# Kernel optimization log

Measured on AMD Instinct MI355X. Metric: run time of the kernel, lower is better.

Reference implementation:

```python
import jax, jax.numpy as jnp
import numpy as np
from jax.scipy.linalg import solve_triangular


def setup_inputs() -> dict:
    key = jax.random.key(0)
    k1, k2 = jax.random.split(key)
    # [K classes, N per class, D features] training embeddings
    src_seq = jax.random.normal(k1, (256, 64, 128), dtype=jnp.float32)
    # [M, D] vectors to project and pairwise-score (clustering inner loop)
    test = jax.random.normal(k2, (8192, 128), dtype=jnp.float32)
    return {"src_seq": src_seq, "test": test}


def _fit_model(src_seq):
    # Faithful port of compute_scatter_matrices + fit_model.
    # S_w, S_b are symmetric PSD, so solve(S_w,S_b) eig is replaced by the
    # equivalent (and differentiable) generalized symmetric eig via Cholesky
    # whitening; A_inverse and psi are invariant to eigvec scaling/order.
    K, N, D = src_seq.shape
    count = K * N
    mean_per_class = src_seq.mean(axis=1)            # [K, D]
    mean = src_seq.mean(axis=(0, 1))                 # [D]
    diff_w = src_seq - mean_per_class[:, None, :]    # [K, N, D]
    diff_b = mean_per_class - mean                   # [K, D]
    S_w = jnp.einsum('knd,kne->de', diff_w, diff_w) / count   # [D, D]
    S_b = (N * jnp.einsum('kd,ke->de', diff_b, diff_b)) / count

    L = jnp.linalg.cholesky(S_w)                     # S_w = L L^T
    # Msym = L^{-1} S_b L^{-T}
    tmp = solve_triangular(L, S_b, lower=True)
    Msym = solve_triangular(L, tmp.T, lower=True).T
    Msym = 0.5 * (Msym + Msym.T)
    evals, U = jnp.linalg.eigh(Msym)
    W = solve_triangular(L, U, lower=True, trans=1)  # W = L^{-T} U, eigvecs of S_w^{-1} S_b

    lambda_b = jnp.sum(W * (S_b @ W), axis=0)        # diag(W^T S_b W)
    lambda_w = jnp.sum(W * (S_w @ W), axis=0)        # diag(W^T S_w W)
    n = float(N)
    # A = W^{-T} diag(sqrt(n/(n-1) * lambda_w))  =>  A^{-1} = diag(1/sqrt(.)) W^T
    A_inverse = (1.0 / jnp.sqrt(n / (n - 1.0) * lambda_w))[:, None] * W.T
    psi = jnp.clip((n - 1.0) / n * (lambda_b / lambda_w) - 1.0 / n, 0.0)
    return A_inverse, mean, psi


def reference(src_seq, test):
    A_inverse, mean, psi = _fit_model(src_seq)
    # latent = A_inverse @ (x - mean), batched over rows
    latent = (test - mean) @ A_inverse.T             # [M, D]
    # Pairwise single-vector probability (calculate_probability_single),
    # vectorized over all (i, j) pairs, in log space:
    # log p(i,j) = -(v_i - v_j)^T diag(psi) (v_i - v_j)
    #             - 0.5 * (D*log(2*pi) + log(||psi||_F))
    D = latent.shape[1]
    q = jnp.sum(psi * latent * latent, axis=1)       # [M]
    G = (latent * psi) @ latent.T                    # [M, M]
    maha = q[:, None] + q[None, :] - 2.0 * G         # [M, M]
    log_div = 0.5 * (D * jnp.log(2.0 * jnp.pi) + jnp.log(jnp.linalg.norm(psi)))
    return -maha - log_div                           # [M, M] pairwise log-prob
```

## Files before the change

### kernel.cpp

```cpp
#include <hip/hip_runtime.h>
#include <math.h>


#define D 128
#define NCLS 256
#define NPC 64
#define MTEST 8192
#define COUNT (NCLS*NPC)

#define fMC    0
#define fMEAN  16384
#define fSCAL  16640
#define fMAT   32768
#define fSWRAW 442368
#define fPART  458752
#define fU     458752
#define fV     983040
#define fQ     1507328
#define fBBF   1515520

#define sP   0
#define sSB  1
#define sP2  2
#define sP3  3
#define sP4  4
#define sZ   5
#define sM1  6
#define sMm  7
#define sC2  8
#define sC4  9
#define sXH  10
#define sT2  11
#define sT3  12
#define sT4  13
#define sT5  14
#define sT10 15
#define sT15 16
#define sT20 17
#define sG0  18
#define sF   23
#define sA1  24

using short8 = __attribute__((ext_vector_type(8))) short;
using f32x4  = __attribute__((ext_vector_type(4))) float;

__device__ inline unsigned short f2bf(float f) {
  unsigned u = __float_as_uint(f);
  unsigned r = u + 0x7FFFu + ((u >> 16) & 1u);
  return (unsigned short)(r >> 16);
}
__device__ inline float bf2f(unsigned short h) {
  return __uint_as_float(((unsigned)h) << 16);
}
__device__ inline float valU(const unsigned short* m, int idx) {
  return bf2f(m[idx]) + bf2f(m[idx + 16384]);
}
__device__ inline void storeDual(unsigned short* m, int idx, float g) {
  unsigned short hb = f2bf(g);
  m[idx] = hb;
  m[16384 + idx] = f2bf(g - bf2f(hb));
}
__device__ inline unsigned short* MS(float* ws, int m) {
  return (unsigned short*)(ws + fMAT) + (size_t)m * 32768;
}
__device__ inline const unsigned short* MSc(const float* ws, int m) {
  return (const unsigned short*)(ws + fMAT) + (size_t)m * 32768;
}

__global__ __launch_bounds__(256) void k_gt_partial(const float* __restrict__ X, float* __restrict__ ws) {
  __shared__ unsigned short xt[128 * 256];
  int b = blockIdx.x, tid = threadIdx.x;
  const float* Xc = X + b * 256 * D;
  for (int idx = tid; idx < 256 * D; idx += 256) {
    int s = idx >> 7, d = idx & 127;
    unsigned byte = ((unsigned)(d * 512 + s * 2)) ^ (((unsigned)(d & 7)) << 4);
    *(unsigned short*)((char*)xt + byte) = f2bf(Xc[idx]);
  }
  {
    int d = tid & 127;
    for (int cc = (tid >> 7); cc < 4; cc += 2) {
      const float* p = Xc + cc * 64 * D + d;
// ... 28 lines not shown
  }
  float* outp = ws + fPART + b * 16384;
  #pragma unroll
  for (int mt = 0; mt < 4; mt++)
    #pragma unroll
    for (int nt = 0; nt < 4; nt++)
      #pragma unroll
      for (int r = 0; r < 4; r++) {
        int row = wr + mt * 16 + (lane >> 4) * 4 + r;
        int col = wc + nt * 16 + (lane & 15);
        outp[row * 128 + col] = acc[mt][nt][r];
      }
}

__global__ void k_reduce(float* __restrict__ ws) {
  int tid = threadIdx.x;
  int idx = blockIdx.x * 256 + tid;
  const float* part = ws + fPART;
  float s = 0.f;
  #pragma unroll 8
  for (int p = 0; p < 64; p++) s += part[p * 16384 + idx];
  ws[fSWRAW + idx] = s;
  if (blockIdx.x == 0 && tid < 128) {
    const unsigned short* McT = (const unsigned short*)ws;
    float m = 0.f;
    for (int k = 0; k < 256; k++) m += bf2f(McT[tid * 256 + k]);
    ws[fMEAN + tid] = m * (1.0f / 256.0f);
  }
}

__global__ __launch_bounds__(256) void k_sb(float* __restrict__ ws) {
  __shared__ float red[4];
  const unsigned short* Mc = (const unsigned short*)ws;
  const float* mv = ws + fMEAN;
  const float* swraw = ws + fSWRAW;
  unsigned short* SB = MS(ws, sSB);
  float* scal = ws + fSCAL;
  int tid = threadIdx.x, b = blockIdx.x;
  int w = tid >> 6, lane = tid & 63;
  int brow = b * 32, wcol = w * 32;
  f32x4 acc[2][2] = {};
  for (int ks = 0; ks < 8; ks++) {
    int kb = ks * 32 + (lane >> 4) * 8;
    short8 af[2], bfv[2];
    #pragma unroll
    for (int mt = 0; mt < 2; mt++) {
      int r = brow + mt * 16 + (lane & 15);
      af[mt] = *(const short8*)(Mc + r * 256 + kb);
    }
    #pragma unroll
    for (int nt = 0; nt < 2; nt++) {
      int c = wcol + nt * 16 + (lane & 15);
      bfv[nt] = *(const short8*)(Mc + c * 256 + kb);
    }
    #pragma unroll
    for (int mt = 0; mt < 2; mt++)
      #pragma unroll
      for (int nt = 0; nt < 2; nt++)
        acc[mt][nt] = __builtin_amdgcn_mfma_f32_16x16x32_bf16(af[mt], bfv[nt], acc[mt][nt], 0, 0, 0);
  }
  float tsum = 0.f;
  #pragma unroll
  for (int mt = 0; mt < 2; mt++)
    #pragma unroll
    for (int nt = 0; nt < 2; nt++)
      #pragma unroll
      for (int r = 0; r < 4; r++) {
        int row = brow + mt * 16 + (lane >> 4) * 4 + r;
        int col = wcol + nt * 16 + (lane & 15);
        int idx = row * 128 + col;
        float g = acc[mt][nt][r] * (1.0f / 256.0f) - mv[row] * mv[col];
        storeDual(SB, idx, g);
        if (row == col)
          tsum += swraw[row * 129] * (1.0f / COUNT) - g - mv[row] * mv[row];
      }
  #pragma unroll
  for (int off = 32; off > 0; off >>= 1) tsum += __shfl_down(tsum, off);
  if (lane == 0) red[w] = tsum;
  __syncthreads();
  if (tid == 0) scal[64 + b] = red[0] + red[1] + red[2] + red[3];
}

__global__ __launch_bounds__(256) void k_swfin(float* __restrict__ ws) {
  float* scal = ws + fSCAL;
  float inv_s = 128.0f / (scal[64] + scal[65] + scal[66] + scal[67]);
  const float* mv = ws + fMEAN;
  const float* swraw = ws + fSWRAW;
  const unsigned short* SB = MS(ws, sSB);
  unsigned short* P = MS(ws, sP);
  int gid = blockIdx.x * 256 + threadIdx.x;
  #pragma unroll
  for (int t = 0; t < 4; t++) {
    int idx = gid * 4 + t;
    int row = idx >> 7, col = idx & 127;
    float sb = valU(SB, idx);
    float s = (swraw[idx] * (1.0f / COUNT) - sb - mv[row] * mv[col]) * inv_s;
    storeDual(P, idx, s - ((row == col) ? 1.0f : 0.0f));
  }
  if (blockIdx.x == 0 && threadIdx.x == 0) {
    scal[1] = inv_s;
    scal[7] = 0.984375f * inv_s;
  }
}

__device__ __forceinline__ void mm_body(
    const unsigned short* __restrict__ A, const unsigned short* __restrict__ B,
    unsigned short* __restrict__ C, const unsigned short* __restrict__ E1,
    float alpha, const float* alpha_ptr, float beta, float delta,
    float* scal, int trace_slot, unsigned short* outBf, int b, float* red) {
  int tid = threadIdx.x;
  int w = tid >> 6, lane = tid & 63;
  int brow = b * 32, wcol = w * 32;
  f32x4 acc[2][2] = {};
  #pragma unroll
  for (int ks = 0; ks < 4; ks++) {
    int kb = ks * 32 + (lane >> 4) * 8;
    short8 ah[2], al[2], bh[2], bl[2];
    #pragma unroll
    for (int mt = 0; mt < 2; mt++) {
      int r = brow + mt * 16 + (lane & 15);
      ah[mt] = *(const short8*)(A + r * 128 + kb);
      al[mt] = *(const short8*)(A + 16384 + r * 128 + kb);
    }
    #pragma unroll
    for (int nt = 0; nt < 2; nt++) {
      int c = wcol + nt * 16 + (lane & 15);
      bh[nt] = *(const short8*)(B + c * 128 + kb);
      bl[nt] = *(const short8*)(B + 16384 + c * 128 + kb);
    }
    #pragma unroll
    for (int mt = 0; mt < 2; mt++)
      #pragma unroll
      for (int nt = 0; nt < 2; nt++) {
        f32x4 a0 = acc[mt][nt];
        a0 = __builtin_amdgcn_mfma_f32_16x16x32_bf16(ah[mt], bh[nt], a0, 0, 0, 0);
        a0 = __builtin_amdgcn_mfma_f32_16x16x32_bf16(al[mt], bh[nt], a0, 0, 0, 0);
        a0 = __builtin_amdgcn_mfma_f32_16x16x32_bf16(ah[mt], bl[nt], a0, 0, 0, 0);
        acc[mt][nt] = a0;
      }
  }
  float aeff = alpha * (alpha_ptr ? alpha_ptr[0] : 1.0f);
  float tsum = 0.0f;
  #pragma unroll
  for (int mt = 0; mt < 2; mt++)
    #pragma unroll
    for (int nt = 0; nt < 2; nt++)
      #pragma unroll
      for (int r = 0; r < 4; r++) {
        int row = brow + mt * 16 + (lane >> 4) * 4 + r;
        int col = wcol + nt * 16 + (lane & 15);
        int idx = row * 128 + col;
        float g = acc[mt][nt][r] * aeff;
        if (E1) g += beta * (bf2f(E1[idx]) + bf2f(E1[16384 + idx]));
        if (row == col) g += delta;
        if (outBf) outBf[idx] = f2bf(g);
        else storeDual(C, idx, g);
        tsum += g * g;
      }
  if (trace_slot >= 0) {
    #pragma unroll
    for (int off = 32; off > 0; off >>= 1) tsum += __shfl_down(tsum, off);
    if (lane == 0) red[w] = tsum;
    __syncthreads();
    if (tid == 0) scal[trace_slot + b] = red[0] + red[1] + red[2] + red[3];
  }
}

__global__ __launch_bounds__(256) void k_mm(
    const unsigned short* A, const unsigned short* B, unsigned short* C,
    const unsigned short* E1, float alpha, const float* alpha_ptr,
    float beta, float delta, float* scal, int trace_slot, unsigned short* outBf) {
  __shared__ float red[4];
  mm_body(A, B, C, E1, alpha, alpha_ptr, beta, delta, scal, trace_slot, outBf, blockIdx.x, red);
}

__global__ __launch_bounds__(256) void k_mm2(
    const unsigned short* A0, const unsigned short* B0, unsigned short* C0,
    const unsigned short* E0, float al0, float be0, float de0,
    const unsigned short* A1, const unsigned short* B1, unsigned short* C1,
    const unsigned short* E1, float al1, float be1, float de1,
    float* scal, int tslot1) {
  __shared__ float red[4];
  int b = blockIdx.x & 3;
  if (blockIdx.x < 4)
    mm_body(A0, B0, C0, E0, al0, nullptr, be0, de0, scal, -1, nullptr, b, red);
  else
    mm_body(A1, B1, C1, E1, al1, nullptr, be1, de1, scal, tslot1, nullptr, b, red);
}

__global__ __launch_bounds__(256) void k_p56z(float* __restrict__ ws) {
  __shared__ float cj[7];
  __shared__ float bt[7];
  float* scal = ws + fSCAL;
  const unsigned short *P = MSc(ws, sP), *P2 = MSc(ws, sP2),
    *P3 = MSc(ws, sP3), *P4 = MSc(ws, sP4);
  unsigned short* Z = MS(ws, sZ);
  int tid = threadIdx.x, b = blockIdx.x;
  float trP8 = scal[60] + scal[61] + scal[62] + scal[63];
  float a = 1.05f * sqrtf(sqrtf(sqrtf(fmaxf(trP8, 1e-30f))));
  a = fminf(a, 0.95f);
  if (tid < 7) {
    const float PI = 3.14159265358979f;
    float s = 0.f;
    for (int i = 0; i < 64; i++) {
      float th = (i + 0.5f) * (PI / 64.0f);
      float x = cosf(th);
      s += (1.0f / sqrtf(1.0f + a * x)) * cosf((float)tid * th);
    }
    cj[tid] = s * (2.0f / 64.0f);
  }
  __syncthreads();
  if (tid == 0) {
    float c0h = 0.5f * cj[0];
    float m0 = c0h - cj[2] + cj[4] - cj[6];
    float m1 = cj[1] - 3.0f * cj[3] + 5.0f * cj[5];
    float m2 = 2.0f * cj[2] - 8.0f * cj[4] + 18.0f * cj[6];
    float m3 = 4.0f * cj[3] - 20.0f * cj[5];
    float m4 = 8.0f * cj[4] - 48.0f * cj[6];
    float m5 = 16.0f * cj[5];
    float m6 = 32.0f * cj[6];
    float ia = 1.0f / a;
    float p = 1.f;
    bt[0] = m0;
    p *= ia; bt[1] = m1 * p;
    p *= ia; bt[2] = m2 * p;
    p *= ia; bt[3] = m3 * p;
    p *= ia; bt[4] = m4 * p;
    p *= ia; bt[5] = m5 * p;
    p *= ia; bt[6] = m6 * p;
  }
  __syncthreads();
  int w = tid >> 6, lane = tid & 63;
  int brow = b * 32, wcol = w * 32;
  f32x4 a5[2][2] = {}, a6[2][2] = {};
  #pragma unroll
  for (int ks = 0; ks < 4; ks++) {
    int kb = ks * 32 + (lane >> 4) * 8;
// ... 33 lines not shown
    #pragma unroll
    for (int nt = 0; nt < 2; nt++)
      #pragma unroll
      for (int r = 0; r < 4; r++) {
        int row = brow + mt * 16 + (lane >> 4) * 4 + r;
        int col = wcol + nt * 16 + (lane & 15);
        int idx = row * 128 + col;
        float dg = (row == col) ? 1.0f : 0.0f;
        float z = bt[0] * dg + bt[1] * valU(P, idx) + bt[2] * valU(P2, idx) +
                  bt[3] * valU(P3, idx) + bt[4] * valU(P4, idx) +
                  bt[5] * a5[mt][nt][r] + bt[6] * a6[mt][nt][r];
        storeDual(Z, idx, z);
      }
}

__device__ inline void interval_cs(const float* scal, float* c0o, float* iho) {
  float trM8 = scal[68] + scal[69] + scal[70] + scal[71];
  float Lam = 1.03f * sqrtf(sqrtf(sqrtf(fmaxf(trM8, 1e-37f))));
  float lo = -0.02f * Lam, hi = Lam;
  *c0o = 0.5f * (hi + lo);
  *iho = 1.0f / (0.5f * (hi - lo));
}

__global__ __launch_bounds__(256) void k_xh_t2(float* __restrict__ ws) {
  __shared__ float cs[2];
  float* scal = ws + fSCAL;
  if (threadIdx.x == 0) {
    float c0, ih;
    interval_cs(scal, &c0, &ih);
    cs[0] = c0; cs[1] = ih;
  }
  __syncthreads();
  float c0 = cs[0], ih = cs[1];
  float a2 = 2.0f * ih * ih, b2 = -4.0f * c0 * ih * ih, g2 = 2.0f * c0 * c0 * ih * ih - 1.0f;
  const unsigned short* Mm = MSc(ws, sMm);
  const unsigned short* C2 = MSc(ws, sC2);
  unsigned short* XH = MS(ws, sXH);
  unsigned short* T2 = MS(ws, sT2);
  int gid = blockIdx.x * 256 + threadIdx.x;
  #pragma unroll
  for (int t = 0; t < 4; t++) {
    int idx = gid * 4 + t;
    int row = idx >> 7, col = idx & 127;
    float m = valU(Mm, idx), c2v = valU(C2, idx);
    float dg = (row == col) ? 1.0f : 0.0f;
    storeDual(XH, idx, ih * m - ih * c0 * dg);
    storeDual(T2, idx, a2 * c2v + b2 * m + g2 * dg);
  }
}

__global__ __launch_bounds__(256) void k_t5g(float* __restrict__ ws) {
  __shared__ float red[4];
  __shared__ float cs[8];
  __shared__ float sat[25];
  __shared__ float sc[25];
  float* scal = ws + fSCAL;
  int tid = threadIdx.x;
  if (blockIdx.x < 4) {
    mm_body(MSc(ws, sT2), MSc(ws, sT3), MS(ws, sT5), MSc(ws, sXH),
            2.0f, nullptr, -1.0f, 0.0f, scal, -1, nullptr, blockIdx.x, red);
    return;
  }
  if (tid == 0) {
    float c0, ih;
    interval_cs(scal, &c0, &ih);
    float inv_s = scal[1];
    float t0 = (1.0f / 63.0f) / inv_s;
    float x0 = fminf(fmaxf((t0 - c0) * ih, -1.0f), 1.0f);
    cs[0] = acosf(x0); cs[1] = x0;
    cs[2] = 0.984375f * inv_s / ih;
  }
  __syncthreads();
  if (tid <= 24) {
    float th = cs[0], x0 = cs[1], SCc = cs[2];
    const float PI = 3.14159265358979f;
// ... 8 lines not shown
    }
    sat[tid] = v;
    sc[tid] = 0.f;
  }
  __syncthreads();
  if (tid == 0) {
    for (int j = 24; j >= 5; --j) {
      int k = j / 5, r = j - 5 * k;
      float aj = sat[j];
      if (r == 0) sc[k * 5] += aj;
      else { sc[k * 5 + r] += 2.0f * aj; sat[5 * k - r] -= aj; }
    }
    for (int r = 0; r < 5; r++) sc[r] += sat[r];
  }
  __syncthreads();
  const unsigned short* XH = MSc(ws, sXH);
  const unsigned short* T2 = MSc(ws, sT2);
  const unsigned short* T3 = MSc(ws, sT3);
  const unsigned short* T4 = MSc(ws, sT4);
  int bg = blockIdx.x - 4;
  int base = bg * 1024 + tid * 4;
  #pragma unroll
  for (int t = 0; t < 4; t++) {
    int idx = base + t;
    int row = idx >> 7, col = idx & 127;
    float dg = (row == col) ? 1.0f : 0.0f;
    float x1 = valU(XH, idx), x2 = valU(T2, idx), x3 = valU(T3, idx), x4 = valU(T4, idx);
    #pragma unroll
    for (int k = 0; k < 5; k++) {
      float g = sc[k * 5 + 0] * dg + sc[k * 5 + 1] * x1 + sc[k * 5 + 2] * x2 +
                sc[k * 5 + 3] * x3 + sc[k * 5 + 4] * x4;
      storeDual(MS(ws, sG0 + k), idx, g);
    }
  }
}

__global__ __launch_bounds__(256) void k_bigF(float* __restrict__ ws) {
  __shared__ float red[4];
  float* scal = ws + fSCAL;
  const unsigned short* As[4] = { MSc(ws, sT5), MSc(ws, sT10), MSc(ws, sT15), MSc(ws, sT20) };
  const unsigned short* Bs[4] = { MSc(ws, sG0 + 1), MSc(ws, sG0 + 2), MSc(ws, sG0 + 3), MSc(ws, sG0 + 4) };
  const unsigned short* G0 = MSc(ws, sG0);
  unsigned short* Fm = MS(ws, sF);
  int tid = threadIdx.x, b = blockIdx.x;
  int w = tid >> 6, lane = tid & 63;
  int brow = b * 32, wcol = w * 32;
  f32x4 acc[2][2] = {};
  for (int p = 0; p < 4; p++) {
    const unsigned short* A = As[p];
    const unsigned short* B = Bs[p];
    #pragma unroll
    for (int ks = 0; ks < 4; ks++) {
      int kb = ks * 32 + (lane >> 4) * 8;
      short8 ah[2], al[2], bh[2], bl[2];
      #pragma unroll
      for (int mt = 0; mt < 2; mt++) {
        int r = brow + mt * 16 + (lane & 15);
// ... 25 lines not shown
    for (int nt = 0; nt < 2; nt++)
      #pragma unroll
      for (int r = 0; r < 4; r++) {
        int row = brow + mt * 16 + (lane >> 4) * 4 + r;
        int col = wcol + nt * 16 + (lane & 15);
        int idx = row * 128 + col;
        float g = acc[mt][nt][r] + valU(G0, idx);
        storeDual(Fm, idx, g);
        tsum += g * g;
      }
  #pragma unroll
  for (int off = 32; off > 0; off >>= 1) tsum += __shfl_down(tsum, off);
  if (lane == 0) red[w] = tsum;
  __syncthreads();
  if (tid == 0) scal[72 + b] = red[0] + red[1] + red[2] + red[3];
}

__global__ __launch_bounds__(256) void k_latent(const float* __restrict__ test, float* __restrict__ ws) {
  __shared__ unsigned short vh[16384];
  __shared__ float qs[128];
  int blk = blockIdx.x, tid = threadIdx.x;
  if (blk == 0 && tid == 0) {
    float* scal = ws + fSCAL;
    float trF2 = fmaxf(scal[72] + scal[73] + scal[74] + scal[75], 1e-30f);
    scal[0] = 0.5f * (128.0f * 1.8378770664093453f + 0.5f * logf(trF2));
  }
  const float* tb = test + blk * 128 * D;
  unsigned short* Vbf = (unsigned short*)(ws + fV);
  if (tid < 128) qs[tid] = 0.f;
  for (int idx = tid; idx < 16384; idx += 256) {
// ... 106 lines not shown
        int col = wc + nt * 16 + (lane & 15);
        float g = acc[mt][nt][r];
        out[(size_t)(bi * 128 + row) * MTEST + (bj * 128 + col)] =
          2.0f * g - qi[row] - qj[col] - ld;
      }
}

extern "C" void kernel_launch(void* const* d_in, const int* in_sizes, int n_in,
                              void* d_out, int out_size, void* d_ws, size_t ws_size,
                              hipStream_t stream) {
  (void)in_sizes; (void)n_in; (void)out_size; (void)ws_size;
  const float* X = (const float*)d_in[0];
  const float* test = (const float*)d_in[1];
  float* out = (float*)d_out;
  float* ws = (float*)d_ws;
  float* scal = ws + fSCAL;
  auto M = [&](int i) -> unsigned short* {
    return (unsigned short*)(ws + fMAT) + (size_t)i * 32768;
  };
  unsigned short* Bbf = (unsigned short*)(ws + fBBF);

  k_gt_partial<<<64, 256, 0, stream>>>(X, ws);
  k_reduce<<<64, 256, 0, stream>>>(ws);
  k_sb<<<4, 256, 0, stream>>>(ws);
  k_swfin<<<16, 256, 0, stream>>>(ws);
  k_mm<<<4, 256, 0, stream>>>(M(sP), M(sP), M(sP2), nullptr, 1.0f, nullptr, 0, 0, scal, -1, nullptr);
  k_mm2<<<8, 256, 0, stream>>>(M(sP2), M(sP), M(sP3), nullptr, 1.0f, 0, 0,
                               M(sP2), M(sP2), M(sP4), nullptr, 1.0f, 0, 0, scal, 60);
  k_p56z<<<4, 256, 0, stream>>>(ws);
  k_mm<<<4, 256, 0, stream>>>(M(sZ), M(sSB), M(sM1), nullptr, 1.0f, nullptr, 0, 0, scal, -1, nullptr);
  k_mm<<<4, 256, 0, stream>>>(M(sM1), M(sZ), M(sMm), nullptr, 1.0f, nullptr, 0, 0, scal, -1, nullptr);
  k_mm<<<4, 256, 0, stream>>>(M(sMm), M(sMm), M(sC2), nullptr, 1.0f, nullptr, 0, 0, scal, -1, nullptr);
  k_mm<<<4, 256, 0, stream>>>(M(sC2), M(sC2), M(sC4), nullptr, 1.0f, nullptr, 0, 0, scal, 68, nullptr);
  k_xh_t2<<<16, 256, 0, stream>>>(ws);
  k_mm2<<<8, 256, 0, stream>>>(M(sXH), M(sT2), M(sT3), M(sXH), 2.0f, -1.0f, 0,
                               M(sT2), M(sT2), M(sT4), nullptr, 2.0f, 0, -1.0f, scal, -1);
  k_t5g<<<20, 256, 0, stream>>>(ws);
  k_mm<<<4, 256, 0, stream>>>(M(sT5), M(sT5), M(sT10), nullptr, 2.0f, nullptr, 0, -1.0f, scal, -1, nullptr);
  k_mm2<<<8, 256, 0, stream>>>(M(sT10), M(sT5), M(sT15), M(sT5), 2.0f, -1.0f, 0,
                               M(sT10), M(sT10), M(sT20), nullptr, 2.0f, 0, -1.0f, scal, -1);
  k_bigF<<<4, 256, 0, stream>>>(ws);
  k_mm<<<4, 256, 0, stream>>>(M(sZ), M(sF), M(sA1), nullptr, 1.0f, nullptr, 0, 0, scal, -1, nullptr);
  k_mm<<<4, 256, 0, stream>>>(M(sA1), M(sZ), nullptr, nullptr, 1.0f, scal + 7, 0, 0, scal, -1, Bbf);
  k_latent<<<64, 256, 0, stream>>>(test, ws);
  k_pair<<<dim3(64, 64), 256, 0, stream>>>(ws, out);
}
```

Measured before the change: 277.8 us.

## Fuse chained small matmuls into fewer kernels with LDS-held intermediates

Merges sequences of dependent 128x128 matrix products (P^2/P^3/P^4, Z*SB*Z, C2/C4, T10/T15/T20, Z*F*Z) into single kernels. Each block recomputes the full first product into shared memory and then computes its row slice of the second product. The trace for the S_w normalisation moves into k_reduce so the S_b and P computations can run in one kernel. This removes many kernel launches and global round trips on the serial fit chain, at the cost of redundant compute per block and large LDS use with only 4 blocks.

Result: slower. 300.5 us (+8.2%).

```diff
diff --git a/kernel.cpp b/kernel.cpp
--- a/kernel.cpp
+++ b/kernel.cpp
@@ -25,10 +25,8 @@
 #define sP3  3
 #define sP4  4
 #define sZ   5
-#define sM1  6
 #define sMm  7
 #define sC2  8
-#define sC4  9
 #define sXH  10
 #define sT2  11
 #define sT3  12
@@ -39,7 +37,6 @@
 #define sT20 17
 #define sG0  18
 #define sF   23
-#define sA1  24
 
 using short8 = __attribute__((ext_vector_type(8))) short;
 using f32x4  = __attribute__((ext_vector_type(4))) float;
@@ -63,8 +60,68 @@
 __device__ inline unsigned short* MS(float* ws, int m) {
   return (unsigned short*)(ws + fMAT) + (size_t)m * 32768;
 }
-__device__ inline const unsigned short* MSc(const float* ws, int m) {
-  return (const unsigned short*)(ws + fMAT) + (size_t)m * 32768;
+__device__ inline short8 lds8(const unsigned short* L, int row, int colk) {
+  unsigned u = ((unsigned)(row * 128 + colk)) ^ (((unsigned)(row & 7)) << 3);
+  return *(const short8*)(L + u);
+}
+__device__ inline void ldsPutDual(unsigned short* L, int row, int col, float g) {
+  unsigned u = ((unsigned)(row * 128 + col)) ^ (((unsigned)(row & 7)) << 3);
+  unsigned short hb = f2bf(g);
+  L[u] = hb;
+  L[16384 + u] = f2bf(g - bf2f(hb));
+}
+
+__device__ float mm_body(const unsigned short* A, const unsigned short* B,
+                         unsigned short* C, const unsigned short* E1,
+                         float alpha, float beta, float delta, int brow) {
+  int tid = threadIdx.x;
+  int w = tid >> 6, lane = tid & 63;
+  int wcol = w * 32;
+  f32x4 acc[2][2] = {};
+  #pragma unroll
+  for (int ks = 0; ks < 4; ks++) {
+    int kb = ks * 32 + (lane >> 4) * 8;
+    short8 ah[2], al[2], bh[2], bl[2];
+    #pragma unroll
+    for (int mt = 0; mt < 2; mt++) {
+      int r = brow + mt * 16 + (lane & 15);
+      ah[mt] = *(const short8*)(A + r * 128 + kb);
+      al[mt] = *(const short8*)(A + 16384 + r * 128 + kb);
+    }
+    #pragma unroll
+    for (int nt = 0; nt < 2; nt++) {
+      int c = wcol + nt * 16 + (lane & 15);
+      bh[nt] = *(const short8*)(B + c * 128 + kb);
+      bl[nt] = *(const short8*)(B + 16384 + c * 128 + kb);
+    }
+    #pragma unroll
+    for (int mt = 0; mt < 2; mt++)
+      #pragma unroll
+      for (int nt = 0; nt < 2; nt++) {
+        f32x4 a0 = acc[mt][nt];
+        a0 = __builtin_amdgcn_mfma_f32_16x16x32_bf16(ah[mt], bh[nt], a0, 0, 0, 0);
+        a0 = __builtin_amdgcn_mfma_f32_16x16x32_bf16(al[mt], bh[nt], a0, 0, 0, 0);
+        a0 = __builtin_amdgcn_mfma_f32_16x16x32_bf16(ah[mt], bl[nt], a0, 0, 0, 0);
+        acc[mt][nt] = a0;
+      }
+  }
+  float tsum = 0.f;
+  #pragma unroll
+  for (int mt = 0; mt < 2; mt++)
+    #pragma unroll
+    for (int nt = 0; nt < 2; nt++)
+      #pragma unroll
+      for (int r = 0; r < 4; r++) {
+        int row = brow + mt * 16 + (lane >> 4) * 4 + r;
+        int col = wcol + nt * 16 + (lane & 15);
+        int idx = row * 128 + col;
+        float g = acc[mt][nt][r] * alpha;
+        if (E1) g += beta * valU(E1, idx);
+        if (row == col) g += delta;
+        storeDual(C, idx, g);
+        tsum += g * g;
+      }
+  return tsum;
 }
 
 __global__ __launch_bounds__(256) void k_gt_partial(const float* __restrict__ X, float* __restrict__ ws) {
@@ -123,6 +180,7 @@
 }
 
 __global__ void k_reduce(float* __restrict__ ws) {
+  __shared__ float red2[4];
   int tid = threadIdx.x;
   int idx = blockIdx.x * 256 + tid;
   const float* part = ws + fPART;
@@ -136,15 +194,35 @@
     for (int k = 0; k < 256; k++) m += bf2f(McT[tid * 256 + k]);
     ws[fMEAN + tid] = m * (1.0f / 256.0f);
   }
-}
-
-__global__ __launch_bounds__(256) void k_sb(float* __restrict__ ws) {
-  __shared__ float red[4];
+  if (blockIdx.x == 1) {
+    float v = 0.f;
+    if (tid < 128) {
+      float gdd = 0.f;
+      for (int p = 0; p < 64; p++) gdd += part[p * 16384 + tid * 129];
+      const unsigned short* McT = (const unsigned short*)ws;
+      float nrm = 0.f;
+      for (int k = 0; k < 256; k++) { float x = bf2f(McT[tid * 256 + k]); nrm += x * x; }
+      v = gdd * (1.0f / COUNT) - nrm * (1.0f / 256.0f);
+    }
+    #pragma unroll
+    for (int off = 32; off > 0; off >>= 1) v += __shfl_down(v, off);
+    if ((tid & 63) == 0) red2[tid >> 6] = v;
+    __syncthreads();
+    if (tid == 0) {
+      float inv_s = 128.0f / (red2[0] + red2[1] + red2[2] + red2[3]);
+      ws[fSCAL + 1] = inv_s;
+      ws[fSCAL + 7] = 0.984375f * inv_s;
+    }
+  }
+}
+
+__global__ __launch_bounds__(256) void k_sbp(float* __restrict__ ws) {
   const unsigned short* Mc = (const unsigned short*)ws;
   const float* mv = ws + fMEAN;
   const float* swraw = ws + fSWRAW;
+  float inv_s = ws[fSCAL + 1];
   unsigned short* SB = MS(ws, sSB);
-  float* scal = ws + fSCAL;
+  unsigned short* P = MS(ws, sP);
   int tid = threadIdx.x, b = blockIdx.x;
   int w = tid >> 6, lane = tid & 63;
   int brow = b * 32, wcol = w * 32;
@@ -168,7 +246,6 @@
       for (int nt = 0; nt < 2; nt++)
         acc[mt][nt] = __builtin_amdgcn_mfma_f32_16x16x32_bf16(af[mt], bfv[nt], acc[mt][nt], 0, 0, 0);
   }
-  float tsum = 0.f;
   #pragma unroll
   for (int mt = 0; mt < 2; mt++)
     #pragma unroll
@@ -180,129 +257,127 @@
         int idx = row * 128 + col;
         float g = acc[mt][nt][r] * (1.0f / 256.0f) - mv[row] * mv[col];
         storeDual(SB, idx, g);
-        if (row == col)
-          tsum += swraw[row * 129] * (1.0f / COUNT) - g - mv[row] * mv[row];
-      }
+        float s = (swraw[idx] * (1.0f / COUNT) - g - mv[row] * mv[col]) * inv_s;
+        storeDual(P, idx, s - ((row == col) ? 1.0f : 0.0f));
+      }
+}
+
+__global__ __launch_bounds__(256) void k_p234(float* __restrict__ ws) {
+  __shared__ unsigned short sL[32768];
+  float* scal = ws + fSCAL;
+  const unsigned short* P = MS(ws, sP);
+  unsigned short* P2 = MS(ws, sP2);
+  unsigned short* P3 = MS(ws, sP3);
+  unsigned short* P4 = MS(ws, sP4);
+  int tid = threadIdx.x, b = blockIdx.x;
+  int w = tid >> 6, lane = tid & 63;
+  int wcol = w * 32, brow = b * 32;
+  {
+    f32x4 acc[8][2] = {};
+    for (int ks = 0; ks < 4; ks++) {
+      int kb = ks * 32 + (lane >> 4) * 8;
+      short8 bh[2], bl[2];
+      #pragma unroll
+      for (int nt = 0; nt < 2; nt++) {
+        int c = wcol + nt * 16 + (lane & 15);
+        bh[nt] = *(const short8*)(P + c * 128 + kb);
+        bl[nt] = *(const short8*)(P + 16384 + c * 128 + kb);
+      }
+      #pragma unroll
+      for (int mt = 0; mt < 8; mt++) {
+        int r = mt * 16 + (lane & 15);
+        short8 ah = *(const short8*)(P + r * 128 + kb);
+        short8 al = *(const short8*)(P + 16384 + r * 128 + kb);
+        #pragma unroll
+        for (int nt = 0; nt < 2; nt++) {
+          f32x4 a0 = acc[mt][nt];
+          a0 = __builtin_amdgcn_mfma_f32_16x16x32_bf16(ah, bh[nt], a0, 0, 0, 0);
+          a0 = __builtin_amdgcn_mfma_f32_16x16x32_bf16(al, bh[nt], a0, 0, 0, 0);
+          a0 = __builtin_amdgcn_mfma_f32_16x16x32_bf16(ah, bl[nt], a0, 0, 0, 0);
+          acc[mt][nt] = a0;
+        }
+      }
+    }
+    #pragma unroll
+    for (int mt = 0; mt < 8; mt++)
+      #pragma unroll
+      for (int nt = 0; nt < 2; nt++)
+        #pragma unroll
+        for (int r = 0; r < 4; r++) {
+          int row = mt * 16 + (lane >> 4) * 4 + r;
+          int col = wcol + nt * 16 + (lane & 15);
+          float g = acc[mt][nt][r];
+          ldsPutDual(sL, row, col, g);
+          storeDual(P2, row * 128 + col, g);
+        }
+  }
+  __syncthreads();
+  float tsum = 0.f;
+  {
+    f32x4 a3[2][2] = {}, a4[2][2] = {};
+    for (int ks = 0; ks < 4; ks++) {
+      int kb = ks * 32 + (lane >> 4) * 8;
+      short8 ah[2], al[2], b3h[2], b3l[2], b4h[2], b4l[2];
+      #pragma unroll
+      for (int mt = 0; mt < 2; mt++) {
+        int r = brow + mt * 16 + (lane & 15);
+        ah[mt] = lds8(sL, r, kb);
+        al[mt] = lds8(sL + 16384, r, kb);
+      }
+      #pragma unroll
+      for (int nt = 0; nt < 2; nt++) {
+        int c = wcol + nt * 16 + (lane & 15);
+        b3h[nt] = *(const short8*)(P + c * 128 + kb);
+        b3l[nt] = *(const short8*)(P + 16384 + c * 128 + kb);
+        b4h[nt] = lds8(sL, c, kb);
+        b4l[nt] = lds8(sL + 16384, c, kb);
+      }
+      #pragma unroll
+      for (int mt = 0; mt < 2; mt++)
+        #pragma unroll
+        for (int nt = 0; nt < 2; nt++) {
+          f32x4 x3 = a3[mt][nt];
+          x3 = __builtin_amdgcn_mfma_f32_16x16x32_bf16(ah[mt], b3h[nt], x3, 0, 0, 0);
+          x3 = __builtin_amdgcn_mfma_f32_16x16x32_bf16(al[mt], b3h[nt], x3, 0, 0, 0);
+          x3 = __builtin_amdgcn_mfma_f32_16x16x32_bf16(ah[mt], b3l[nt], x3, 0, 0, 0);
+          a3[mt][nt] = x3;
+          f32x4 x4 = a4[mt][nt];
+          x4 = __builtin_amdgcn_mfma_f32_16x16x32_bf16(ah[mt], b4h[nt], x4, 0, 0, 0);
+          x4 = __builtin_amdgcn_mfma_f32_16x16x32_bf16(al[mt], b4h[nt], x4, 0, 0, 0);
+          x4 = __builtin_amdgcn_mfma_f32_16x16x32_bf16(ah[mt], b4l[nt], x4, 0, 0, 0);
+          a4[mt][nt] = x4;
+        }
+    }
+    #pragma unroll
+    for (int mt = 0; mt < 2; mt++)
+      #pragma unroll
+      for (int nt = 0; nt < 2; nt++)
+        #pragma unroll
+        for (int r = 0; r < 4; r++) {
+          int row = brow + mt * 16 + (lane >> 4) * 4 + r;
+          int col = wcol + nt * 16 + (lane & 15);
+          int idx = row * 128 + col;
+          storeDual(P3, idx, a3[mt][nt][r]);
+          float g4 = a4[mt][nt][r];
+          storeDual(P4, idx, g4);
+          tsum += g4 * g4;
+        }
+  }
   #pragma unroll
   for (int off = 32; off > 0; off >>= 1) tsum += __shfl_down(tsum, off);
+  __syncthreads();
+  float* red = (float*)sL;
   if (lane == 0) red[w] = tsum;
   __syncthreads();
-  if (tid == 0) scal[64 + b] = red[0] + red[1] + red[2] + red[3];
-}
-
-__global__ __launch_bounds__(256) void k_swfin(float* __restrict__ ws) {
-  float* scal = ws + fSCAL;
-  float inv_s = 128.0f / (scal[64] + scal[65] + scal[66] + scal[67]);
-  const float* mv = ws + fMEAN;
-  const float* swraw = ws + fSWRAW;
-  const unsigned short* SB = MS(ws, sSB);
-  unsigned short* P = MS(ws, sP);
-  int gid = blockIdx.x * 256 + threadIdx.x;
-  #pragma unroll
-  for (int t = 0; t < 4; t++) {
-    int idx = gid * 4 + t;
-    int row = idx >> 7, col = idx & 127;
-    float sb = valU(SB, idx);
-    float s = (swraw[idx] * (1.0f / COUNT) - sb - mv[row] * mv[col]) * inv_s;
-    storeDual(P, idx, s - ((row == col) ? 1.0f : 0.0f));
-  }
-  if (blockIdx.x == 0 && threadIdx.x == 0) {
-    scal[1] = inv_s;
-    scal[7] = 0.984375f * inv_s;
-  }
-}
-
-__device__ __forceinline__ void mm_body(
-    const unsigned short* __restrict__ A, const unsigned short* __restrict__ B,
-    unsigned short* __restrict__ C, const unsigned short* __restrict__ E1,
-    float alpha, const float* alpha_ptr, float beta, float delta,
-    float* scal, int trace_slot, unsigned short* outBf, int b, float* red) {
-  int tid = threadIdx.x;
-  int w = tid >> 6, lane = tid & 63;
-  int brow = b * 32, wcol = w * 32;
-  f32x4 acc[2][2] = {};
-  #pragma unroll
-  for (int ks = 0; ks < 4; ks++) {
-    int kb = ks * 32 + (lane >> 4) * 8;
-    short8 ah[2], al[2], bh[2], bl[2];
-    #pragma unroll
-    for (int mt = 0; mt < 2; mt++) {
-      int r = brow + mt * 16 + (lane & 15);
-      ah[mt] = *(const short8*)(A + r * 128 + kb);
-      al[mt] = *(const short8*)(A + 16384 + r * 128 + kb);
-    }
-    #pragma unroll
-    for (int nt = 0; nt < 2; nt++) {
-      int c = wcol + nt * 16 + (lane & 15);
-      bh[nt] = *(const short8*)(B + c * 128 + kb);
-      bl[nt] = *(const short8*)(B + 16384 + c * 128 + kb);
-    }
-    #pragma unroll
-    for (int mt = 0; mt < 2; mt++)
-      #pragma unroll
-      for (int nt = 0; nt < 2; nt++) {
-        f32x4 a0 = acc[mt][nt];
-        a0 = __builtin_amdgcn_mfma_f32_16x16x32_bf16(ah[mt], bh[nt], a0, 0, 0, 0);
-        a0 = __builtin_amdgcn_mfma_f32_16x16x32_bf16(al[mt], bh[nt], a0, 0, 0, 0);
-        a0 = __builtin_amdgcn_mfma_f32_16x16x32_bf16(ah[mt], bl[nt], a0, 0, 0, 0);
-        acc[mt][nt] = a0;
-      }
-  }
-  float aeff = alpha * (alpha_ptr ? alpha_ptr[0] : 1.0f);
-  float tsum = 0.0f;
-  #pragma unroll
-  for (int mt = 0; mt < 2; mt++)
-    #pragma unroll
-    for (int nt = 0; nt < 2; nt++)
-      #pragma unroll
-      for (int r = 0; r < 4; r++) {
-        int row = brow + mt * 16 + (lane >> 4) * 4 + r;
-        int col = wcol + nt * 16 + (lane & 15);
-        int idx = row * 128 + col;
-        float g = acc[mt][nt][r] * aeff;
-        if (E1) g += beta * (bf2f(E1[idx]) + bf2f(E1[16384 + idx]));
-        if (row == col) g += delta;
-        if (outBf) outBf[idx] = f2bf(g);
-        else storeDual(C, idx, g);
-        tsum += g * g;
-      }
-  if (trace_slot >= 0) {
-    #pragma unroll
-    for (int off = 32; off > 0; off >>= 1) tsum += __shfl_down(tsum, off);
-    if (lane == 0) red[w] = tsum;
-    __syncthreads();
-    if (tid == 0) scal[trace_slot + b] = red[0] + red[1] + red[2] + red[3];
-  }
-}
-
-__global__ __launch_bounds__(256) void k_mm(
-    const unsigned short* A, const unsigned short* B, unsigned short* C,
-    const unsigned short* E1, float alpha, const float* alpha_ptr,
-    float beta, float delta, float* scal, int trace_slot, unsigned short* outBf) {
-  __shared__ float red[4];
-  mm_body(A, B, C, E1, alpha, alpha_ptr, beta, delta, scal, trace_slot, outBf, blockIdx.x, red);
-}
-
-__global__ __launch_bounds__(256) void k_mm2(
-    const unsigned short* A0, const unsigned short* B0, unsigned short* C0,
-    const unsigned short* E0, float al0, float be0, float de0,
-    const unsigned short* A1, const unsigned short* B1, unsigned short* C1,
-    const unsigned short* E1, float al1, float be1, float de1,
-    float* scal, int tslot1) {
-  __shared__ float red[4];
-  int b = blockIdx.x & 3;
-  if (blockIdx.x < 4)
-    mm_body(A0, B0, C0, E0, al0, nullptr, be0, de0, scal, -1, nullptr, b, red);
-  else
-    mm_body(A1, B1, C1, E1, al1, nullptr, be1, de1, scal, tslot1, nullptr, b, red);
-}
-
-__global__ __launch_bounds__(256) void k_p56z(float* __restrict__ ws) {
+  if (tid == 0) scal[60 + b] = red[0] + red[1] + red[2] + red[3];
+}
+
+__global__ __launch_bounds__(256) void k_z(float* __restrict__ ws) {
   __shared__ float cj[7];
   __shared__ float bt[7];
   float* scal = ws + fSCAL;
-  const unsigned short *P = MSc(ws, sP), *P2 = MSc(ws, sP2),
-    *P3 = MSc(ws, sP3), *P4 = MSc(ws, sP4);
+  const unsigned short *P = MS(ws, sP), *P2 = MS(ws, sP2),
+    *P3 = MS(ws, sP3), *P4 = MS(ws, sP4);
   unsigned short* Z = MS(ws, sZ);
   int tid = threadIdx.x, b = blockIdx.x;
   float trP8 = scal[60] + scal[61] + scal[62] + scal[63];
@@ -328,8 +403,7 @@
     float m4 = 8.0f * cj[4] - 48.0f * cj[6];
     float m5 = 16.0f * cj[5];
     float m6 = 32.0f * cj[6];
-    float ia = 1.0f / a;
-    float p = 1.f;
+    float ia = 1.0f / a, p = 1.f;
     bt[0] = m0;
     p *= ia; bt[1] = m1 * p;
     p *= ia; bt[2] = m2 * p;
@@ -393,6 +467,189 @@
       }
 }
 
+__global__ __launch_bounds__(256) void k_msb(float* __restrict__ ws) {
+  __shared__ unsigned short sL[32768];
+  const unsigned short* Z = MS(ws, sZ);
+  const unsigned short* SB = MS(ws, sSB);
+  unsigned short* Mm = MS(ws, sMm);
+  int tid = threadIdx.x, b = blockIdx.x;
+  int w = tid >> 6, lane = tid & 63;
+  int wcol = w * 32, brow = b * 32;
+  {
+    f32x4 acc[8][2] = {};
+    for (int ks = 0; ks < 4; ks++) {
+      int kb = ks * 32 + (lane >> 4) * 8;
+      short8 bh[2], bl[2];
+      #pragma unroll
+      for (int nt = 0; nt < 2; nt++) {
+        int c = wcol + nt * 16 + (lane & 15);
+        bh[nt] = *(const short8*)(SB + c * 128 + kb);
+        bl[nt] = *(const short8*)(SB + 16384 + c * 128 + kb);
+      }
+      #pragma unroll
+      for (int mt = 0; mt < 8; mt++) {
+        int r = mt * 16 + (lane & 15);
+        short8 ah = *(const short8*)(Z + r * 128 + kb);
+        short8 al = *(const short8*)(Z + 16384 + r * 128 + kb);
+        #pragma unroll
+        for (int nt = 0; nt < 2; nt++) {
+          f32x4 a0 = acc[mt][nt];
+          a0 = __builtin_amdgcn_mfma_f32_16x16x32_bf16(ah, bh[nt], a0, 0, 0, 0);
+          a0 = __builtin_amdgcn_mfma_f32_16x16x32_bf16(al, bh[nt], a0, 0, 0, 0);
+          a0 = __builtin_amdgcn_mfma_f32_16x16x32_bf16(ah, bl[nt], a0, 0, 0, 0);
+          acc[mt][nt] = a0;
+        }
+      }
+    }
+    #pragma unroll
+    for (int mt = 0; mt < 8; mt++)
+      #pragma unroll
+      for (int nt = 0; nt < 2; nt++)
+        #pragma unroll
+        for (int r = 0; r < 4; r++) {
+          int row = mt * 16 + (lane >> 4) * 4 + r;
+          int col = wcol + nt * 16 + (lane & 15);
+          ldsPutDual(sL, row, col, acc[mt][nt][r]);
+        }
+  }
+  __syncthreads();
+  {
+    f32x4 acc[2][2] = {};
+    for (int ks = 0; ks < 4; ks++) {
+      int kb = ks * 32 + (lane >> 4) * 8;
+      short8 ah[2], al[2], bh[2], bl[2];
+      #pragma unroll
+      for (int mt = 0; mt < 2; mt++) {
+        int r = brow + mt * 16 + (lane & 15);
+        ah[mt] = lds8(sL, r, kb);
+        al[mt] = lds8(sL + 16384, r, kb);
+      }
+      #pragma unroll
+      for (int nt = 0; nt < 2; nt++) {
+        int c = wcol + nt * 16 + (lane & 15);
+        bh[nt] = *(const short8*)(Z + c * 128 + kb);
+        bl[nt] = *(const short8*)(Z + 16384 + c * 128 + kb);
+      }
+      #pragma unroll
+      for (int mt = 0; mt < 2; mt++)
+        #pragma unroll
+        for (int nt = 0; nt < 2; nt++) {
+          f32x4 a0 = acc[mt][nt];
+          a0 = __builtin_amdgcn_mfma_f32_16x16x32_bf16(ah[mt], bh[nt], a0, 0, 0, 0);
+          a0 = __builtin_amdgcn_mfma_f32_16x16x32_bf16(al[mt], bh[nt], a0, 0, 0, 0);
+          a0 = __builtin_amdgcn_mfma_f32_16x16x32_bf16(ah[mt], bl[nt], a0, 0, 0, 0);
+          acc[mt][nt] = a0;
+        }
+    }
+    #pragma unroll
+    for (int mt = 0; mt < 2; mt++)
+      #pragma unroll
+      for (int nt = 0; nt < 2; nt++)
+        #pragma unroll
+        for (int r = 0; r < 4; r++) {
+          int row = brow + mt * 16 + (lane >> 4) * 4 + r;
+          int col = wcol + nt * 16 + (lane & 15);
+          storeDual(Mm, row * 128 + col, acc[mt][nt][r]);
+        }
+  }
+}
+
+__global__ __launch_bounds__(256) void k_c24(float* __restrict__ ws) {
+  __shared__ unsigned short sL[32768];
+  float* scal = ws + fSCAL;
+  const unsigned short* Mm = MS(ws, sMm);
+  unsigned short* C2 = MS(ws, sC2);
+  int tid = threadIdx.x, b = blockIdx.x;
+  int w = tid >> 6, lane = tid & 63;
+  int wcol = w * 32, brow = b * 32;
+  {
+    f32x4 acc[8][2] = {};
+    for (int ks = 0; ks < 4; ks++) {
+      int kb = ks * 32 + (lane >> 4) * 8;
+      short8 bh[2], bl[2];
+      #pragma unroll
+      for (int nt = 0; nt < 2; nt++) {
+        int c = wcol + nt * 16 + (lane & 15);
+        bh[nt] = *(const short8*)(Mm + c * 128 + kb);
+        bl[nt] = *(const short8*)(Mm + 16384 + c * 128 + kb);
+      }
+      #pragma unroll
+      for (int mt = 0; mt < 8; mt++) {
+        int r = mt * 16 + (lane & 15);
+        short8 ah = *(const short8*)(Mm + r * 128 + kb);
+        short8 al = *(const short8*)(Mm + 16384 + r * 128 + kb);
+        #pragma unroll
+        for (int nt = 0; nt < 2; nt++) {
+          f32x4 a0 = acc[mt][nt];
+          a0 = __builtin_amdgcn_mfma_f32_16x16x32_bf16(ah, bh[nt], a0, 0, 0, 0);
+          a0 = __builtin_amdgcn_mfma_f32_16x16x32_bf16(al, bh[nt], a0, 0, 0, 0);
+          a0 = __builtin_amdgcn_mfma_f32_16x16x32_bf16(ah, bl[nt], a0, 0, 0, 0);
+          acc[mt][nt] = a0;
+        }
+      }
+    }
+    #pragma unroll
+    for (int mt = 0; mt < 8; mt++)
+      #pragma unroll
+      for (int nt = 0; nt < 2; nt++)
+        #pragma unroll
+        for (int r = 0; r < 4; r++) {
+          int row = mt * 16 + (lane >> 4) * 4 + r;
+          int col = wcol + nt * 16 + (lane & 15);
+          float g = acc[mt][nt][r];
+          ldsPutDual(sL, row, col, g);
+          storeDual(C2, row * 128 + col, g);
+        }
+  }
+  __syncthreads();
+  float tsum = 0.f;
+  {
+    f32x4 acc[2][2] = {};
+    for (int ks = 0; ks < 4; ks++) {
+      int kb = ks * 32 + (lane >> 4) * 8;
+      short8 ah[2], al[2], bh[2], bl[2];
+      #pragma unroll
+      for (int mt = 0; mt < 2; mt++) {
+        int r = brow + mt * 16 + (lane & 15);
+        ah[mt] = lds8(sL, r, kb);
+        al[mt] = lds8(sL + 16384, r, kb);
+      }
+      #pragma unroll
+      for (int nt = 0; nt < 2; nt++) {
+        int c = wcol + nt * 16 + (lane & 15);
+        bh[nt] = lds8(sL, c, kb);
+        bl[nt] = lds8(sL + 16384, c, kb);
+      }
+      #pragma unroll
+      for (int mt = 0; mt < 2; mt++)
+        #pragma unroll
+        for (int nt = 0; nt < 2; nt++) {
+          f32x4 a0 = acc[mt][nt];
+          a0 = __builtin_amdgcn_mfma_f32_16x16x32_bf16(ah[mt], bh[nt], a0, 0, 0, 0);
+          a0 = __builtin_amdgcn_mfma_f32_16x16x32_bf16(al[mt], bh[nt], a0, 0, 0, 0);
+          a0 = __builtin_amdgcn_mfma_f32_16x16x32_bf16(ah[mt], bl[nt], a0, 0, 0, 0);
+          acc[mt][nt] = a0;
+        }
+    }
+    #pragma unroll
+    for (int mt = 0; mt < 2; mt++)
+      #pragma unroll
+      for (int nt = 0; nt < 2; nt++)
+        #pragma unroll
+        for (int r = 0; r < 4; r++) {
+          float g = acc[mt][nt][r];
+          tsum += g * g;
+        }
+  }
+  #pragma unroll
+  for (int off = 32; off > 0; off >>= 1) tsum += __shfl_down(tsum, off);
+  __syncthreads();
+  float* red = (float*)sL;
+  if (lane == 0) red[w] = tsum;
+  __syncthreads();
+  if (tid == 0) scal[68 + b] = red[0] + red[1] + red[2] + red[3];
+}
+
 __device__ inline void interval_cs(const float* scal, float* c0o, float* iho) {
   float trM8 = scal[68] + scal[69] + scal[70] + scal[71];
   float Lam = 1.03f * sqrtf(sqrtf(sqrtf(fmaxf(trM8, 1e-37f))));
@@ -412,8 +669,8 @@
   __syncthreads();
   float c0 = cs[0], ih = cs[1];
   float a2 = 2.0f * ih * ih, b2 = -4.0f * c0 * ih * ih, g2 = 2.0f * c0 * c0 * ih * ih - 1.0f;
-  const unsigned short* Mm = MSc(ws, sMm);
-  const unsigned short* C2 = MSc(ws, sC2);
+  const unsigned short* Mm = MS(ws, sMm);
+  const unsigned short* C2 = MS(ws, sC2);
   unsigned short* XH = MS(ws, sXH);
   unsigned short* T2 = MS(ws, sT2);
   int gid = blockIdx.x * 256 + threadIdx.x;
@@ -428,16 +685,25 @@
   }
 }
 
+__global__ __launch_bounds__(256) void k_t34(float* __restrict__ ws) {
+  const unsigned short* XH = MS(ws, sXH);
+  const unsigned short* T2 = MS(ws, sT2);
+  if (blockIdx.x < 4) {
+    mm_body(XH, T2, MS(ws, sT3), XH, 2.0f, -1.0f, 0.0f, blockIdx.x * 32);
+  } else {
+    mm_body(T2, T2, MS(ws, sT4), nullptr, 2.0f, 0.0f, -1.0f, (blockIdx.x - 4) * 32);
+  }
+}
+
 __global__ __launch_bounds__(256) void k_t5g(float* __restrict__ ws) {
-  __shared__ float red[4];
   __shared__ float cs[8];
   __shared__ float sat[25];
   __shared__ float sc[25];
   float* scal = ws + fSCAL;
   int tid = threadIdx.x;
   if (blockIdx.x < 4) {
-    mm_body(MSc(ws, sT2), MSc(ws, sT3), MS(ws, sT5), MSc(ws, sXH),
-            2.0f, nullptr, -1.0f, 0.0f, scal, -1, nullptr, blockIdx.x, red);
+    mm_body(MS(ws, sT3), MS(ws, sT2), MS(ws, sT5), MS(ws, sXH),
+            2.0f, -1.0f, 0.0f, blockIdx.x * 32);
     return;
   }
   if (tid == 0) {
@@ -476,10 +742,10 @@
     for (int r = 0; r < 5; r++) sc[r] += sat[r];
   }
   __syncthreads();
-  const unsigned short* XH = MSc(ws, sXH);
-  const unsigned short* T2 = MSc(ws, sT2);
-  const unsigned short* T3 = MSc(ws, sT3);
-  const unsigned short* T4 = MSc(ws, sT4);
+  const unsigned short* XH = MS(ws, sXH);
+  const unsigned short* T2 = MS(ws, sT2);
+  const unsigned short* T3 = MS(ws, sT3);
+  const unsigned short* T4 = MS(ws, sT4);
   int bg = blockIdx.x - 4;
   int base = bg * 1024 + tid * 4;
   #pragma unroll
@@ -497,12 +763,111 @@
   }
 }
 
+__global__ __launch_bounds__(256) void k_t101520(float* __restrict__ ws) {
+  __shared__ unsigned short sL[32768];
+  const unsigned short* T5 = MS(ws, sT5);
+  unsigned short* T10 = MS(ws, sT10);
+  unsigned short* T15 = MS(ws, sT15);
+  unsigned short* T20 = MS(ws, sT20);
+  int tid = threadIdx.x, b = blockIdx.x;
+  int w = tid >> 6, lane = tid & 63;
+  int wcol = w * 32, brow = b * 32;
+  {
+    f32x4 acc[8][2] = {};
+    for (int ks = 0; ks < 4; ks++) {
+      int kb = ks * 32 + (lane >> 4) * 8;
+      short8 bh[2], bl[2];
+      #pragma unroll
+      for (int nt = 0; nt < 2; nt++) {
+        int c = wcol + nt * 16 + (lane & 15);
+        bh[nt] = *(const short8*)(T5 + c * 128 + kb);
+        bl[nt] = *(const short8*)(T5 + 16384 + c * 128 + kb);
+      }
+      #pragma unroll
+      for (int mt = 0; mt < 8; mt++) {
+        int r = mt * 16 + (lane & 15);
+        short8 ah = *(const short8*)(T5 + r * 128 + kb);
+        short8 al = *(const short8*)(T5 + 16384 + r * 128 + kb);
+        #pragma unroll
+        for (int nt = 0; nt < 2; nt++) {
+          f32x4 a0 = acc[mt][nt];
+          a0 = __builtin_amdgcn_mfma_f32_16x16x32_bf16(ah, bh[nt], a0, 0, 0, 0);
+          a0 = __builtin_amdgcn_mfma_f32_16x16x32_bf16(al, bh[nt], a0, 0, 0, 0);
+          a0 = __builtin_amdgcn_mfma_f32_16x16x32_bf16(ah, bl[nt], a0, 0, 0, 0);
+          acc[mt][nt] = a0;
+        }
+      }
+    }
+    #pragma unroll
+    for (int mt = 0; mt < 8; mt++)
+      #pragma unroll
+      for (int nt = 0; nt < 2; nt++)
+        #pragma unroll
+        for (int r = 0; r < 4; r++) {
+          int row = mt * 16 + (lane >> 4) * 4 + r;
+          int col = wcol + nt * 16 + (lane & 15);
+          float g = 2.0f * acc[mt][nt][r] - ((row == col) ? 1.0f : 0.0f);
+          ldsPutDual(sL, row, col, g);
+          storeDual(T10, row * 128 + col, g);
+        }
+  }
+  __syncthreads();
+  {
+    f32x4 a15[2][2] = {}, a20[2][2] = {};
+    for (int ks = 0; ks < 4; ks++) {
+      int kb = ks * 32 + (lane >> 4) * 8;
+      short8 ah[2], al[2], b5h[2], b5l[2], bth[2], btl[2];
+      #pragma unroll
+      for (int mt = 0; mt < 2; mt++) {
+        int r = brow + mt * 16 + (lane & 15);
+        ah[mt] = lds8(sL, r, kb);
+        al[mt] = lds8(sL + 16384, r, kb);
+      }
+      #pragma unroll
+      for (int nt = 0; nt < 2; nt++) {
+        int c = wcol + nt * 16 + (lane & 15);
+        b5h[nt] = *(const short8*)(T5 + c * 128 + kb);
+        b5l[nt] = *(const short8*)(T5 + 16384 + c * 128 + kb);
+        bth[nt] = lds8(sL, c, kb);
+        btl[nt] = lds8(sL + 16384, c, kb);
+      }
+      #pragma unroll
+      for (int mt = 0; mt < 2; mt++)
+        #pragma unroll
+        for (int nt = 0; nt < 2; nt++) {
+          f32x4 x = a15[mt][nt];
+          x = __builtin_amdgcn_mfma_f32_16x16x32_bf16(ah[mt], b5h[nt], x, 0, 0, 0);
+          x = __builtin_amdgcn_mfma_f32_16x16x32_bf16(al[mt], b5h[nt], x, 0, 0, 0);
+          x = __builtin_amdgcn_mfma_f32_16x16x32_bf16(ah[mt], b5l[nt], x, 0, 0, 0);
+          a15[mt][nt] = x;
+          f32x4 y = a20[mt][nt];
+          y = __builtin_amdgcn_mfma_f32_16x16x32_bf16(ah[mt], bth[nt], y, 0, 0, 0);
+          y = __builtin_amdgcn_mfma_f32_16x16x32_bf16(al[mt], bth[nt], y, 0, 0, 0);
+          y = __builtin_amdgcn_mfma_f32_16x16x32_bf16(ah[mt], btl[nt], y, 0, 0, 0);
+          a20[mt][nt] = y;
+        }
+    }
+    #pragma unroll
+    for (int mt = 0; mt < 2; mt++)
+      #pragma unroll
+      for (int nt = 0; nt < 2; nt++)
+        #pragma unroll
+        for (int r = 0; r < 4; r++) {
+          int row = brow + mt * 16 + (lane >> 4) * 4 + r;
+          int col = wcol + nt * 16 + (lane & 15);
+          int idx = row * 128 + col;
+          storeDual(T15, idx, 2.0f * a15[mt][nt][r] - valU(T5, idx));
+          storeDual(T20, idx, 2.0f * a20[mt][nt][r] - ((row == col) ? 1.0f : 0.0f));
+        }
+  }
+}
+
 __global__ __launch_bounds__(256) void k_bigF(float* __restrict__ ws) {
   __shared__ float red[4];
   float* scal = ws + fSCAL;
-  const unsigned short* As[4] = { MSc(ws, sT5), MSc(ws, sT10), MSc(ws, sT15), MSc(ws, sT20) };
-  const unsigned short* Bs[4] = { MSc(ws, sG0 + 1), MSc(ws, sG0 + 2), MSc(ws, sG0 + 3), MSc(ws, sG0 + 4) };
-  const unsigned short* G0 = MSc(ws, sG0);
+  const unsigned short* As[4] = { MS(ws, sT5), MS(ws, sT10), MS(ws, sT15), MS(ws, sT20) };
+  const unsigned short* Bs[4] = { MS(ws, sG0 + 1), MS(ws, sG0 + 2), MS(ws, sG0 + 3), MS(ws, sG0 + 4) };
+  const unsigned short* G0 = MS(ws, sG0);
   unsigned short* Fm = MS(ws, sF);
   int tid = threadIdx.x, b = blockIdx.x;
   int w = tid >> 6, lane = tid & 63;
@@ -558,6 +923,94 @@
   if (lane == 0) red[w] = tsum;
   __syncthreads();
   if (tid == 0) scal[72 + b] = red[0] + red[1] + red[2] + red[3];
+}
+
+__global__ __launch_bounds__(256) void k_zfb(float* __restrict__ ws) {
+  __shared__ unsigned short sL[32768];
+  const unsigned short* Z = MS(ws, sZ);
+  const unsigned short* Fm = MS(ws, sF);
+  unsigned short* Bbf = (unsigned short*)(ws + fBBF);
+  float aeff = ws[fSCAL + 7];
+  int tid = threadIdx.x, b = blockIdx.x;
+  int w = tid >> 6, lane = tid & 63;
+  int wcol = w * 32, brow = b * 32;
+  {
+    f32x4 acc[8][2] = {};
+    for (int ks = 0; ks < 4; ks++) {
+      int kb = ks * 32 + (lane >> 4) * 8;
+      short8 bh[2], bl[2];
+      #pragma unroll
+      for (int nt = 0; nt < 2; nt++) {
+        int c = wcol + nt * 16 + (lane & 15);
+        bh[nt] = *(const short8*)(Fm + c * 128 + kb);
+        bl[nt] = *(const short8*)(Fm + 16384 + c * 128 + kb);
+      }
+      #pragma unroll
+      for (int mt = 0; mt < 8; mt++) {
+        int r = mt * 16 + (lane & 15);
+        short8 ah = *(const short8*)(Z + r * 128 + kb);
+        short8 al = *(const short8*)(Z + 16384 + r * 128 + kb);
+        #pragma unroll
+        for (int nt = 0; nt < 2; nt++) {
+          f32x4 a0 = acc[mt][nt];
+          a0 = __builtin_amdgcn_mfma_f32_16x16x32_bf16(ah, bh[nt], a0, 0, 0, 0);
+          a0 = __builtin_amdgcn_mfma_f32_16x16x32_bf16(al, bh[nt], a0, 0, 0, 0);
+          a0 = __builtin_amdgcn_mfma_f32_16x16x32_bf16(ah, bl[nt], a0, 0, 0, 0);
+          acc[mt][nt] = a0;
+        }
+      }
+    }
+    #pragma unroll
+    for (int mt = 0; mt < 8; mt++)
+      #pragma unroll
+      for (int nt = 0; nt < 2; nt++)
+        #pragma unroll
+        for (int r = 0; r < 4; r++) {
+          int row = mt * 16 + (lane >> 4) * 4 + r;
+          int col = wcol + nt * 16 + (lane & 15);
+          ldsPutDual(sL, row, col, acc[mt][nt][r]);
+        }
+  }
+  __syncthreads();
+  {
+    f32x4 acc[2][2] = {};
+    for (int ks = 0; ks < 4; ks++) {
+      int kb = ks * 32 + (lane >> 4) * 8;
+      short8 ah[2], al[2], bh[2], bl[2];
+      #pragma unroll
+      for (int mt = 0; mt < 2; mt++) {
+        int r = brow + mt * 16 + (lane & 15);
+        ah[mt] = lds8(sL, r, kb);
+        al[mt] = lds8(sL + 16384, r, kb);
+      }
+      #pragma unroll
+      for (int nt = 0; nt < 2; nt++) {
+        int c = wcol + nt * 16 + (lane & 15);
+        bh[nt] = *(const short8*)(Z + c * 128 + kb);
+        bl[nt] = *(const short8*)(Z + 16384 + c * 128 + kb);
+      }
+      #pragma unroll
+      for (int mt = 0; mt < 2; mt++)
+        #pragma unroll
+        for (int nt = 0; nt < 2; nt++) {
+          f32x4 a0 = acc[mt][nt];
+          a0 = __builtin_amdgcn_mfma_f32_16x16x32_bf16(ah[mt], bh[nt], a0, 0, 0, 0);
+          a0 = __builtin_amdgcn_mfma_f32_16x16x32_bf16(al[mt], bh[nt], a0, 0, 0, 0);
+          a0 = __builtin_amdgcn_mfma_f32_16x16x32_bf16(ah[mt], bl[nt], a0, 0, 0, 0);
+          acc[mt][nt] = a0;
+        }
+    }
+    #pragma unroll
+    for (int mt = 0; mt < 2; mt++)
+      #pragma unroll
+      for (int nt = 0; nt < 2; nt++)
+        #pragma unroll
+        for (int r = 0; r < 4; r++) {
+          int row = brow + mt * 16 + (lane >> 4) * 4 + r;
+          int col = wcol + nt * 16 + (lane & 15);
+          Bbf[row * 128 + col] = f2bf(acc[mt][nt][r] * aeff);
+        }
+  }
 }
 
 __global__ __launch_bounds__(256) void k_latent(const float* __restrict__ test, float* __restrict__ ws) {
@@ -694,34 +1147,20 @@
   const float* test = (const float*)d_in[1];
   float* out = (float*)d_out;
   float* ws = (float*)d_ws;
-  float* scal = ws + fSCAL;
-  auto M = [&](int i) -> unsigned short* {
-    return (unsigned short*)(ws + fMAT) + (size_t)i * 32768;
-  };
-  unsigned short* Bbf = (unsigned short*)(ws + fBBF);
 
   k_gt_partial<<<64, 256, 0, stream>>>(X, ws);
   k_reduce<<<64, 256, 0, stream>>>(ws);
-  k_sb<<<4, 256, 0, stream>>>(ws);
-  k_swfin<<<16, 256, 0, stream>>>(ws);
-  k_mm<<<4, 256, 0, stream>>>(M(sP), M(sP), M(sP2), nullptr, 1.0f, nullptr, 0, 0, scal, -1, nullptr);
-  k_mm2<<<8, 256, 0, stream>>>(M(sP2), M(sP), M(sP3), nullptr, 1.0f, 0, 0,
-                               M(sP2), M(sP2), M(sP4), nullptr, 1.0f, 0, 0, scal, 60);
-  k_p56z<<<4, 256, 0, stream>>>(ws);
-  k_mm<<<4, 256, 0, stream>>>(M(sZ), M(sSB), M(sM1), nullptr, 1.0f, nullptr, 0, 0, scal, -1, nullptr);
-  k_mm<<<4, 256, 0, stream>>>(M(sM1), M(sZ), M(sMm), nullptr, 1.0f, nullptr, 0, 0, scal, -1, nullptr);
-  k_mm<<<4, 256, 0, stream>>>(M(sMm), M(sMm), M(sC2), nullptr, 1.0f, nullptr, 0, 0, scal, -1, nullptr);
-  k_mm<<<4, 256, 0, stream>>>(M(sC2), M(sC2), M(sC4), nullptr, 1.0f, nullptr, 0, 0, scal, 68, nullptr);
+  k_sbp<<<4, 256, 0, stream>>>(ws);
+  k_p234<<<4, 256, 0, stream>>>(ws);
+  k_z<<<4, 256, 0, stream>>>(ws);
+  k_msb<<<4, 256, 0, stream>>>(ws);
+  k_c24<<<4, 256, 0, stream>>>(ws);
   k_xh_t2<<<16, 256, 0, stream>>>(ws);
-  k_mm2<<<8, 256, 0, stream>>>(M(sXH), M(sT2), M(sT3), M(sXH), 2.0f, -1.0f, 0,
-                               M(sT2), M(sT2), M(sT4), nullptr, 2.0f, 0, -1.0f, scal, -1);
+  k_t34<<<8, 256, 0, stream>>>(ws);
   k_t5g<<<20, 256, 0, stream>>>(ws);
-  k_mm<<<4, 256, 0, stream>>>(M(sT5), M(sT5), M(sT10), nullptr, 2.0f, nullptr, 0, -1.0f, scal, -1, nullptr);
-  k_mm2<<<8, 256, 0, stream>>>(M(sT10), M(sT5), M(sT15), M(sT5), 2.0f, -1.0f, 0,
-                               M(sT10), M(sT10), M(sT20), nullptr, 2.0f, 0, -1.0f, scal, -1);
+  k_t101520<<<4, 256, 0, stream>>>(ws);
   k_bigF<<<4, 256, 0, stream>>>(ws);
-  k_mm<<<4, 256, 0, stream>>>(M(sZ), M(sF), M(sA1), nullptr, 1.0f, nullptr, 0, 0, scal, -1, nullptr);
-  k_mm<<<4, 256, 0, stream>>>(M(sA1), M(sZ), nullptr, nullptr, 1.0f, scal + 7, 0, 0, scal, -1, Bbf);
+  k_zfb<<<4, 256, 0, stream>>>(ws);
   k_latent<<<64, 256, 0, stream>>>(test, ws);
   k_pair<<<dim3(64, 64), 256, 0, stream>>>(ws, out);
 }
```
